# Kernel optimization log

Measured on AMD Instinct MI355X. Metric: run time of the kernel, lower is better.

## Reference

```python
import jax, jax.numpy as jnp
import numpy as np

N_NODES = 50000
N_EDGES = 800000
IN_CH = 128
HID = 128


def setup_inputs() -> dict:
    key = jax.random.key(0)
    ks = jax.random.split(key, 8)
    s = 0.05
    x = jax.random.normal(ks[0], (N_NODES, IN_CH), dtype=jnp.float32)
    edge_index = jax.random.randint(ks[1], (2, N_EDGES), 0, N_NODES, dtype=jnp.int64)
    W1l = jax.random.normal(ks[2], (IN_CH, HID), dtype=jnp.float32) * s
    W1r = jax.random.normal(ks[3], (IN_CH, HID), dtype=jnp.float32) * s
    b1 = jnp.zeros((HID,), dtype=jnp.float32)
    W2l = jax.random.normal(ks[4], (HID, HID), dtype=jnp.float32) * s
    W2r = jax.random.normal(ks[5], (HID, HID), dtype=jnp.float32) * s
    b2 = jnp.zeros((HID,), dtype=jnp.float32)
    Wout = jax.random.normal(ks[6], (HID, 2), dtype=jnp.float32) * s
    bout = jnp.zeros((2,), dtype=jnp.float32)
    return {"x": x, "edge_index": edge_index, "W1l": W1l, "W1r": W1r, "b1": b1,
            "W2l": W2l, "W2r": W2r, "b2": b2, "Wout": Wout, "bout": bout}


def _mean_aggr(h, src, dst, n_nodes):
    # mean of neighbor (source) features per destination node (PyG SAGEConv default)
    msg_sum = jax.ops.segment_sum(h[src], dst, num_segments=n_nodes)  # [N, D]
    deg = jax.ops.segment_sum(jnp.ones((src.shape[0],), dtype=h.dtype), dst,
                              num_segments=n_nodes)  # [N]
    return msg_sum / jnp.maximum(deg, 1.0)[:, None]


def _sage_conv(h, src, dst, Wl, Wr, b, n_nodes):
    aggr = _mean_aggr(h, src, dst, n_nodes)
    return aggr @ Wl + h @ Wr + b


def reference(x, edge_index, W1l, W1r, b1, W2l, W2r, b2, Wout, bout):
    n = x.shape[0]
    src, dst = edge_index[0], edge_index[1]
    h = jax.nn.relu(_sage_conv(x, src, dst, W1l, W1r, b1, n))
    # dropout is identity in inference mode
    h = jax.nn.relu(_sage_conv(h, src, dst, W2l, W2r, b2, n))
    logits = h @ Wout + bout
    return (logits, h)
```

## Files before the change

kernel.cpp:

```cpp
#include <hip/hip_runtime.h>

#define NN 50000
#define NE 800000
#define CH 128
#define CAP 64

#define NBLK 256
#define EPB (NE / NBLK)
#define HWORDS (NN / 2)

#define WTP_BLK 256
#define CAST_BLK ((NN * (CH / 2) / 4 + 255) / 256)

typedef __attribute__((ext_vector_type(8))) short short8;
typedef __attribute__((ext_vector_type(4))) float float4a;
typedef __attribute__((ext_vector_type(4))) float fltx4;
typedef __attribute__((ext_vector_type(4))) unsigned untx4;

#define DEG_OFF  0
#define CSR_OFF  50048
#define XB_OFF   1650048
#define AGB_OFF  4850048
#define H1B_OFF  8050048
#define WTP_OFF  11250048
#define BH_OFF   AGB_OFF

static __device__ __forceinline__ unsigned short f2b(float f) {
    unsigned u = __float_as_uint(f);
    unsigned r = u + 0x7fff + ((u >> 16) & 1);
    return (unsigned short)(r >> 16);
}

__global__ __launch_bounds__(256) void k_count(
    const int* __restrict__ eidx, unsigned* __restrict__ bh) {
    __shared__ unsigned h[HWORDS];
    for (int i = threadIdx.x; i < HWORDS; i += 256) h[i] = 0;
    __syncthreads();
    int b = blockIdx.x;
    const int* srcp = eidx + (size_t)b * EPB;
    const int* dstp = eidx + NE + (size_t)b * EPB;
    for (int i = threadIdx.x; i < EPB; i += 256) {
        int s = srcp[i];
        int d = dstp[i];
        if ((unsigned)d < NN && (unsigned)s < NN)
            atomicAdd(&h[d >> 1], 1u << ((d & 1) * 16));
    }
    __syncthreads();
    unsigned* out = bh + (size_t)b * HWORDS;
    for (int i = threadIdx.x; i < HWORDS; i += 256) out[i] = h[i];
}

__global__ __launch_bounds__(256) void k_scan(
    unsigned* __restrict__ bh, int* __restrict__ deg) {
    int i = blockIdx.x * 256 + threadIdx.x;
    if (i >= HWORDS) return;
    unsigned lo = 0, hi = 0;
    for (int b = 0; b < NBLK; ++b) {
        unsigned v = bh[(size_t)b * HWORDS + i];
        bh[(size_t)b * HWORDS + i] = lo | (hi << 16);
        lo += v & 0xffffu;
        hi += v >> 16;
    }
    deg[i * 2]     = (int)lo;
    deg[i * 2 + 1] = (int)hi;
}

__global__ __launch_bounds__(256) void k_place(
    const int* __restrict__ eidx, const unsigned* __restrict__ bh,
    unsigned short* __restrict__ csr) {
    __shared__ unsigned h[HWORDS];
    for (int i = threadIdx.x; i < HWORDS; i += 256) h[i] = 0;
    __syncthreads();
    int b = blockIdx.x;
    const int* srcp = eidx + (size_t)b * EPB;
    const int* dstp = eidx + NE + (size_t)b * EPB;
    const unsigned* base = bh + (size_t)b * HWORDS;
    for (int i = threadIdx.x; i < EPB; i += 256) {
        int s = srcp[i];
        int d = dstp[i];
        if ((unsigned)d < NN && (unsigned)s < NN) {
            int sh = (d & 1) * 16;
            unsigned prev = atomicAdd(&h[d >> 1], 1u << sh);
            unsigned rank = (prev >> sh) & 0xffffu;
            unsigned bs = (base[d >> 1] >> sh) & 0xffffu;
            int slot = min((int)(bs + rank), CAP - 1);
            csr[(size_t)d * CAP + slot] = (unsigned short)s;
        }
    }
}

__global__ __launch_bounds__(256) void k_prep(
    const float* __restrict__ W1l, const float* __restrict__ W1r,
    const float* __restrict__ W2l, const float* __restrict__ W2r,
    unsigned short* __restrict__ wtp,
    const float* __restrict__ x, unsigned* __restrict__ xb) {
    int b = blockIdx.x;
    if (b < WTP_BLK) {
        int i = b * 256 + threadIdx.x;
        int layer = i >> 15;
        int li = i & 32767;
        int e = li & 7, lane = (li >> 3) & 63, j = (li >> 9) & 7, kt = li >> 12;
        int ln = lane & 15, quad = lane >> 4;
        int n = j * 16 + ln;
        int k = kt * 32 + quad * 8 + e;
        const float* Wl = layer ? W2l : W1l;
        const float* Wr = layer ? W2r : W1r;
        float v = (k < 128) ? Wl[k * 128 + n] : Wr[(k - 128) * 128 + n];
        __builtin_nontemporal_store(f2b(v), &wtp[(size_t)layer * 32768 + li]);
    } else {
        int gid = (b - WTP_BLK) * 256 + threadIdx.x;
        if (gid < NN * (CH / 2) / 4) {
            fltx4 v0 = __builtin_nontemporal_load((const fltx4*)x + gid * 2);
            fltx4 v1 = __builtin_nontemporal_load((const fltx4*)x + gid * 2 + 1);
            untx4 o;
            o.x = (unsigned)f2b(v0.x) | ((unsigned)f2b(v0.y) << 16);
            o.y = (unsigned)f2b(v0.z) | ((unsigned)f2b(v0.w) << 16);
            o.z = (unsigned)f2b(v1.x) | ((unsigned)f2b(v1.y) << 16);
            o.w = (unsigned)f2b(v1.z) | ((unsigned)f2b(v1.w) << 16);
            __builtin_nontemporal_store(o, (untx4*)xb + gid);
        }
    }
}

static __device__ __forceinline__ void acc8(float* acc, uint4 v) {
    acc[0] += __uint_as_float(v.x << 16); acc[1] += __uint_as_float(v.x & 0xffff0000u);
    acc[2] += __uint_as_float(v.y << 16); acc[3] += __uint_as_float(v.y & 0xffff0000u);
    acc[4] += __uint_as_float(v.z << 16); acc[5] += __uint_as_float(v.z & 0xffff0000u);
    acc[6] += __uint_as_float(v.w << 16); acc[7] += __uint_as_float(v.w & 0xffff0000u);
}

__global__ __launch_bounds__(256) void k_gather4(
    const int* __restrict__ deg, const unsigned short* __restrict__ csr,
    const uint4* __restrict__ featb, uint4* __restrict__ aggrb) {
    int wave = (blockIdx.x * 256 + threadIdx.x) >> 6;
    int lane = threadIdx.x & 63;
    if (wave >= NN) return;
    int d = min(deg[wave], CAP);
    const unsigned short* row = csr + (size_t)wave * CAP;
    int g = lane >> 4;
    int c = lane & 15;

    float acc[8];
    #pragma unroll
    for (int e = 0; e < 8; ++e) acc[e] = 0.0f;

    int i0 = 0;
    for (; i0 + 16 <= d; i0 += 16) {
        int s1 = row[i0 + g];
        int s2 = row[i0 + 4 + g];
        int s3 = row[i0 + 8 + g];
        int s4 = row[i0 + 12 + g];
        uint4 v1 = featb[(size_t)s1 * 16 + c];
        uint4 v2 = featb[(size_t)s2 * 16 + c];
        uint4 v3 = featb[(size_t)s3 * 16 + c];
        uint4 v4 = featb[(size_t)s4 * 16 + c];
        acc8(acc, v1); acc8(acc, v2); acc8(acc, v3); acc8(acc, v4);
    }
    for (; i0 + 8 <= d; i0 += 8) {
        int s1 = row[i0 + g];
        int s2 = row[i0 + 4 + g];
        uint4 v1 = featb[(size_t)s1 * 16 + c];
        uint4 v2 = featb[(size_t)s2 * 16 + c];
        acc8(acc, v1); acc8(acc, v2);
    }
    if (i0 < d) {
        int n1 = i0 + g, n2 = i0 + 4 + g;
        int s1 = (n1 < d) ? (int)row[n1] : 0;
        int s2 = (n2 < d) ? (int)row[n2] : 0;
        uint4 v1 = featb[(size_t)s1 * 16 + c];
        uint4 v2 = featb[(size_t)s2 * 16 + c];
        if (n1 < d) acc8(acc, v1);
        if (n2 < d) acc8(acc, v2);
    }

    #pragma unroll
    for (int e = 0; e < 8; ++e) {
        acc[e] += __shfl_xor(acc[e], 32, 64);
        acc[e] += __shfl_xor(acc[e], 16, 64);
    }
    if (lane < 16) {
        float s = 1.0f / (float)(d > 1 ? d : 1);
        uint4 o;
        o.x = (unsigned)f2b(acc[0] * s) | ((unsigned)f2b(acc[1] * s) << 16);
        o.y = (unsigned)f2b(acc[2] * s) | ((unsigned)f2b(acc[3] * s) << 16);
        o.z = (unsigned)f2b(acc[4] * s) | ((unsigned)f2b(acc[5] * s) << 16);
        o.w = (unsigned)f2b(acc[6] * s) | ((unsigned)f2b(acc[7] * s) << 16);
        aggrb[(size_t)wave * 16 + c] = o;
    }
}

template <bool BF16OUT>
__global__ __launch_bounds__(256) void k_layer_mfma(
    const short* __restrict__ aggrb, const short* __restrict__ hinb,
    const short* __restrict__ wtp, const float* __restrict__ bias,
    float* __restrict__ outf, unsigned short* __restrict__ outb,
    const float* __restrict__ Wout, const float* __restrict__ bout,
    float* __restrict__ logits) {
    int lane = threadIdx.x & 63;
    int wid = threadIdx.x >> 6;
    int m0 = blockIdx.x * 64 + wid * 16;
    int ln = lane & 15;
    int quad = lane >> 4;
    int m = m0 + ln;
    int mc = min(m, NN - 1);

    float4a acc[8];
    #pragma unroll
    for (int j = 0; j < 8; ++j) acc[j] = (float4a){0.0f, 0.0f, 0.0f, 0.0f};

    #pragma unroll
    for (int kt = 0; kt < 8; ++kt) {
        const short* arow = (kt < 4 ? aggrb : hinb) + (size_t)mc * CH + (kt & 3) * 32 + quad * 8;
        short8 av = *(const short8*)arow;
        const short* bk = wtp + (size_t)kt * 4096 + lane * 8;
        #pragma unroll
        for (int j = 0; j < 8; ++j) {
            short8 bv = *(const short8*)(bk + j * 512);
            acc[j] = __builtin_amdgcn_mfma_f32_16x16x32_bf16(av, bv, acc[j], 0, 0, 0);
        }
    }

    float p0[4], p1[4];
    #pragma unroll
    for (int r = 0; r < 4; ++r) { p0[r] = 0.0f; p1[r] = 0.0f; }

    #pragma unroll
    for (int j = 0; j < 8; ++j) {
        int col = j * 16 + ln;
        float bj = bias[col];
        float w0 = 0.0f, w1 = 0.0f;
        if (!BF16OUT) { w0 = Wout[col * 2]; w1 = Wout[col * 2 + 1]; }
        #pragma unroll
        for (int r = 0; r < 4; ++r) {
            int row = m0 + quad * 4 + r;
            float v = fmaxf(acc[j][r] + bj, 0.0f);
            if (row < NN) {
                if (BF16OUT) outb[(size_t)row * CH + col] = f2b(v);
                else         outf[(size_t)row * CH + col] = v;
            }
            if (!BF16OUT) { p0[r] = fmaf(v, w0, p0[r]); p1[r] = fmaf(v, w1, p1[r]); }
        }
    }

    if (!BF16OUT) {
        #pragma unroll
        for (int r = 0; r < 4; ++r) {
            #pragma unroll
            for (int off = 1; off < 16; off <<= 1) {
                p0[r] += __shfl_xor(p0[r], off, 64);
                p1[r] += __shfl_xor(p1[r], off, 64);
            }
        }
        if (ln == 0) {
            float b0 = bout[0], b1 = bout[1];
            #pragma unroll
            for (int r = 0; r < 4; ++r) {
                int row = m0 + quad * 4 + r;
                if (row < NN) {
                    logits[row * 2 + 0] = p0[r] + b0;
                    logits[row * 2 + 1] = p1[r] + b1;
                }
            }
        }
    }
}

extern "C" void kernel_launch(void* const* d_in, const int* in_sizes, int n_in,
                              void* d_out, int out_size, void* d_ws, size_t ws_size,
                              hipStream_t stream) {
    const float* x    = (const float*)d_in[0];
    const int*   eidx = (const int*)d_in[1];
    const float* W1l  = (const float*)d_in[2];
    const float* W1r  = (const float*)d_in[3];
    const float* b1   = (const float*)d_in[4];
    const float* W2l  = (const float*)d_in[5];
    const float* W2r  = (const float*)d_in[6];
    const float* b2   = (const float*)d_in[7];
    const float* Wout = (const float*)d_in[8];
    const float* bout = (const float*)d_in[9];

    float* out    = (float*)d_out;
    float* ws     = (float*)d_ws;
    int*   deg    = (int*)ws;
    unsigned short* csr = (unsigned short*)(ws + CSR_OFF);
    unsigned* xb  = (unsigned*)(ws + XB_OFF);
    unsigned* agb = (unsigned*)(ws + AGB_OFF);
    unsigned* h1b = (unsigned*)(ws + H1B_OFF);
    unsigned* bh  = (unsigned*)(ws + BH_OFF);
    unsigned short* wtp = (unsigned short*)(ws + WTP_OFF);
    float* logits = out;
    float* hout   = out + 100000;

    k_count<<<NBLK, 256, 0, stream>>>(eidx, bh);
    k_scan<<<(HWORDS + 255) / 256, 256, 0, stream>>>(bh, deg);
    k_place<<<NBLK, 256, 0, stream>>>(eidx, bh, csr);

    k_prep<<<WTP_BLK + CAST_BLK, 256, 0, stream>>>(W1l, W1r, W2l, W2r, wtp, x, xb);

    k_gather4<<<(NN + 3) / 4, 256, 0, stream>>>(deg, csr, (const uint4*)xb, (uint4*)agb);
    k_layer_mfma<true><<<(NN + 63) / 64, 256, 0, stream>>>(
        (const short*)agb, (const short*)xb, (const short*)wtp, b1,
        nullptr, (unsigned short*)h1b, nullptr, nullptr, nullptr);

    k_gather4<<<(NN + 3) / 4, 256, 0, stream>>>(deg, csr, (const uint4*)h1b, (uint4*)agb);
    k_layer_mfma<false><<<(NN + 63) / 64, 256, 0, stream>>>(
        (const short*)agb, (const short*)h1b, (const short*)(wtp + 32768), b2,
        hout, nullptr, Wout, bout, logits);
}
```

Before: 251.1 us.

## Split column scan into two levels and store per-edge ranks for flat placement

The per-node prefix scan over 256 block histograms is split into two passes: eight groups of 32 blocks scanned in parallel, then a short scan over the group partials. This is meant to shorten the serial dependency chain of the old single-pass scan, which only launched about 98 blocks. k_count now records each edge's local rank, so k_place becomes a flat one-thread-per-edge kernel with no shared-memory histogram or atomics. In exchange it adds an extra launch, workspace for the ranks and partials, and more global reads in placement.

```diff
diff --git a/kernel.cpp b/kernel.cpp
--- a/kernel.cpp
+++ b/kernel.cpp
@@ -8,6 +8,7 @@
 #define NBLK 256
 #define EPB (NE / NBLK)
 #define HWORDS (NN / 2)
+#define NGRP 8
 
 #define WTP_BLK 256
 #define CAST_BLK ((NN * (CH / 2) / 4 + 255) / 256)
@@ -23,7 +24,9 @@
 #define AGB_OFF  4850048
 #define H1B_OFF  8050048
 #define WTP_OFF  11250048
-#define BH_OFF   AGB_OFF
+#define BH_OFF   11283456
+#define RNK_OFF  17683456
+#define PART_OFF 18083456
 
 static __device__ __forceinline__ unsigned short f2b(float f) {
     unsigned u = __float_as_uint(f);
@@ -32,32 +35,56 @@
 }
 
 __global__ __launch_bounds__(256) void k_count(
-    const int* __restrict__ eidx, unsigned* __restrict__ bh) {
+    const int* __restrict__ eidx, unsigned* __restrict__ bh,
+    unsigned short* __restrict__ rnk) {
     __shared__ unsigned h[HWORDS];
     for (int i = threadIdx.x; i < HWORDS; i += 256) h[i] = 0;
     __syncthreads();
     int b = blockIdx.x;
-    const int* srcp = eidx + (size_t)b * EPB;
-    const int* dstp = eidx + NE + (size_t)b * EPB;
+    int ebase = b * EPB;
     for (int i = threadIdx.x; i < EPB; i += 256) {
-        int s = srcp[i];
-        int d = dstp[i];
-        if ((unsigned)d < NN && (unsigned)s < NN)
-            atomicAdd(&h[d >> 1], 1u << ((d & 1) * 16));
+        int e = ebase + i;
+        int s = eidx[e];
+        int d = eidx[NE + e];
+        unsigned r = 0xffffu;
+        if ((unsigned)d < NN && (unsigned)s < NN) {
+            int sh = (d & 1) * 16;
+            unsigned prev = atomicAdd(&h[d >> 1], 1u << sh);
+            r = (prev >> sh) & 0xffffu;
+        }
+        rnk[e] = (unsigned short)r;
     }
     __syncthreads();
     unsigned* out = bh + (size_t)b * HWORDS;
     for (int i = threadIdx.x; i < HWORDS; i += 256) out[i] = h[i];
 }
 
-__global__ __launch_bounds__(256) void k_scan(
-    unsigned* __restrict__ bh, int* __restrict__ deg) {
+__global__ __launch_bounds__(256) void k_scanA(
+    unsigned* __restrict__ bh, unsigned* __restrict__ part) {
+    int i = blockIdx.x * 256 + threadIdx.x;
+    if (i >= HWORDS) return;
+    int g = blockIdx.y;
+    unsigned lo = 0, hi = 0;
+    size_t base = (size_t)g * 32 * HWORDS + i;
+    #pragma unroll 4
+    for (int b = 0; b < 32; ++b) {
+        unsigned v = bh[base + (size_t)b * HWORDS];
+        bh[base + (size_t)b * HWORDS] = lo | (hi << 16);
+        lo += v & 0xffffu;
+        hi += v >> 16;
+    }
+    part[(size_t)g * HWORDS + i] = lo | (hi << 16);
+}
+
+__global__ __launch_bounds__(256) void k_scanB(
+    unsigned* __restrict__ part, int* __restrict__ deg) {
     int i = blockIdx.x * 256 + threadIdx.x;
     if (i >= HWORDS) return;
     unsigned lo = 0, hi = 0;
-    for (int b = 0; b < NBLK; ++b) {
-        unsigned v = bh[(size_t)b * HWORDS + i];
-        bh[(size_t)b * HWORDS + i] = lo | (hi << 16);
+    #pragma unroll
+    for (int g = 0; g < NGRP; ++g) {
+        unsigned v = part[(size_t)g * HWORDS + i];
+        part[(size_t)g * HWORDS + i] = lo | (hi << 16);
         lo += v & 0xffffu;
         hi += v >> 16;
     }
@@ -67,26 +94,20 @@
 
 __global__ __launch_bounds__(256) void k_place(
     const int* __restrict__ eidx, const unsigned* __restrict__ bh,
+    const unsigned* __restrict__ part, const unsigned short* __restrict__ rnk,
     unsigned short* __restrict__ csr) {
-    __shared__ unsigned h[HWORDS];
-    for (int i = threadIdx.x; i < HWORDS; i += 256) h[i] = 0;
-    __syncthreads();
-    int b = blockIdx.x;
-    const int* srcp = eidx + (size_t)b * EPB;
-    const int* dstp = eidx + NE + (size_t)b * EPB;
-    const unsigned* base = bh + (size_t)b * HWORDS;
-    for (int i = threadIdx.x; i < EPB; i += 256) {
-        int s = srcp[i];
-        int d = dstp[i];
-        if ((unsigned)d < NN && (unsigned)s < NN) {
-            int sh = (d & 1) * 16;
-            unsigned prev = atomicAdd(&h[d >> 1], 1u << sh);
-            unsigned rank = (prev >> sh) & 0xffffu;
-            unsigned bs = (base[d >> 1] >> sh) & 0xffffu;
-            int slot = min((int)(bs + rank), CAP - 1);
-            csr[(size_t)d * CAP + slot] = (unsigned short)s;
-        }
-    }
+    int e = blockIdx.x * 256 + threadIdx.x;
+    if (e >= NE) return;
+    int s = eidx[e];
+    int d = eidx[NE + e];
+    if ((unsigned)d >= NN || (unsigned)s >= NN) return;
+    int b = e / EPB;
+    int sh = (d & 1) * 16;
+    unsigned lb = (bh[(size_t)b * HWORDS + (d >> 1)] >> sh) & 0xffffu;
+    unsigned gb = (part[(size_t)(b >> 5) * HWORDS + (d >> 1)] >> sh) & 0xffffu;
+    unsigned r = rnk[e];
+    int slot = min((int)(gb + lb + r), CAP - 1);
+    csr[(size_t)d * CAP + slot] = (unsigned short)s;
 }
 
 __global__ __launch_bounds__(256) void k_prep(
@@ -286,14 +307,18 @@
     unsigned* xb  = (unsigned*)(ws + XB_OFF);
     unsigned* agb = (unsigned*)(ws + AGB_OFF);
     unsigned* h1b = (unsigned*)(ws + H1B_OFF);
+    unsigned short* wtp = (unsigned short*)(ws + WTP_OFF);
     unsigned* bh  = (unsigned*)(ws + BH_OFF);
-    unsigned short* wtp = (unsigned short*)(ws + WTP_OFF);
+    unsigned short* rnk = (unsigned short*)(ws + RNK_OFF);
+    unsigned* part = (unsigned*)(ws + PART_OFF);
     float* logits = out;
     float* hout   = out + 100000;
 
-    k_count<<<NBLK, 256, 0, stream>>>(eidx, bh);
-    k_scan<<<(HWORDS + 255) / 256, 256, 0, stream>>>(bh, deg);
-    k_place<<<NBLK, 256, 0, stream>>>(eidx, bh, csr);
+    k_count<<<NBLK, 256, 0, stream>>>(eidx, bh, rnk);
+    dim3 sgrid((HWORDS + 255) / 256, NGRP);
+    k_scanA<<<sgrid, 256, 0, stream>>>(bh, part);
+    k_scanB<<<(HWORDS + 255) / 256, 256, 0, stream>>>(part, deg);
+    k_place<<<(NE + 255) / 256, 256, 0, stream>>>(eidx, bh, part, rnk, csr);
 
     k_prep<<<WTP_BLK + CAST_BLK, 256, 0, stream>>>(W1l, W1r, W2l, W2r, wtp, x, xb);
 
```

After: 248.1 us. Within noise of the previous version (-1.2%).

## Fuse gather into MFMA layer kernel and restructure CSR build with stored ranks

Applied to the files above, without the earlier changes.

The neighbor mean-aggregation is fused into the MFMA layer kernel. Each wave gathers 16 rows into LDS and the block then runs the GEMM from LDS, so the aggregated bf16 buffer never goes to global memory and two launches disappear. CSR construction now records per-edge ranks in the count pass, which lets the place step run as a flat per-edge pass merged with the weight and x prep kernel. The histogram block count drops from 256 to 64, cutting scan traffic at the cost of less count parallelism. The risk is that fused blocks cover only 64 nodes with serial per-wave gathers, which may limit occupancy and latency hiding.

```diff
diff --git a/kernel.cpp b/kernel.cpp
--- a/kernel.cpp
+++ b/kernel.cpp
@@ -5,12 +5,13 @@
 #define CH 128
 #define CAP 64
 
-#define NBLK 256
+#define NBLK 64
 #define EPB (NE / NBLK)
 #define HWORDS (NN / 2)
 
+#define PLACE_BLK (NE / 256)
 #define WTP_BLK 256
-#define CAST_BLK ((NN * (CH / 2) / 4 + 255) / 256)
+#define CAST_BLK (NN * (CH / 2) / 4 / 256)
 
 typedef __attribute__((ext_vector_type(8))) short short8;
 typedef __attribute__((ext_vector_type(4))) float float4a;
@@ -20,10 +21,10 @@
 #define DEG_OFF  0
 #define CSR_OFF  50048
 #define XB_OFF   1650048
-#define AGB_OFF  4850048
-#define H1B_OFF  8050048
-#define WTP_OFF  11250048
-#define BH_OFF   AGB_OFF
+#define H1B_OFF  4850048
+#define WTP_OFF  8050048
+#define BH_OFF   8083456
+#define RNK_OFF  9683456
 
 static __device__ __forceinline__ unsigned short f2b(float f) {
     unsigned u = __float_as_uint(f);
@@ -32,18 +33,24 @@
 }
 
 __global__ __launch_bounds__(256) void k_count(
-    const int* __restrict__ eidx, unsigned* __restrict__ bh) {
+    const int* __restrict__ eidx, unsigned* __restrict__ bh,
+    unsigned short* __restrict__ rnk) {
     __shared__ unsigned h[HWORDS];
     for (int i = threadIdx.x; i < HWORDS; i += 256) h[i] = 0;
     __syncthreads();
     int b = blockIdx.x;
-    const int* srcp = eidx + (size_t)b * EPB;
-    const int* dstp = eidx + NE + (size_t)b * EPB;
+    int ebase = b * EPB;
     for (int i = threadIdx.x; i < EPB; i += 256) {
-        int s = srcp[i];
-        int d = dstp[i];
-        if ((unsigned)d < NN && (unsigned)s < NN)
-            atomicAdd(&h[d >> 1], 1u << ((d & 1) * 16));
+        int e = ebase + i;
+        int s = eidx[e];
+        int d = eidx[NE + e];
+        unsigned r = 0xffffu;
+        if ((unsigned)d < NN && (unsigned)s < NN) {
+            int sh = (d & 1) * 16;
+            unsigned prev = atomicAdd(&h[d >> 1], 1u << sh);
+            r = (prev >> sh) & 0xffffu;
+        }
+        rnk[e] = (unsigned short)r;
     }
     __syncthreads();
     unsigned* out = bh + (size_t)b * HWORDS;
@@ -55,48 +62,37 @@
     int i = blockIdx.x * 256 + threadIdx.x;
     if (i >= HWORDS) return;
     unsigned lo = 0, hi = 0;
+    #pragma unroll 8
     for (int b = 0; b < NBLK; ++b) {
         unsigned v = bh[(size_t)b * HWORDS + i];
         bh[(size_t)b * HWORDS + i] = lo | (hi << 16);
         lo += v & 0xffffu;
         hi += v >> 16;
     }
-    deg[i * 2]     = (int)lo;
-    deg[i * 2 + 1] = (int)hi;
-}
-
-__global__ __launch_bounds__(256) void k_place(
+    int2 o; o.x = (int)lo; o.y = (int)hi;
+    *(int2*)&deg[i * 2] = o;
+}
+
+__global__ __launch_bounds__(256) void k_place_prep(
     const int* __restrict__ eidx, const unsigned* __restrict__ bh,
-    unsigned short* __restrict__ csr) {
-    __shared__ unsigned h[HWORDS];
-    for (int i = threadIdx.x; i < HWORDS; i += 256) h[i] = 0;
-    __syncthreads();
-    int b = blockIdx.x;
-    const int* srcp = eidx + (size_t)b * EPB;
-    const int* dstp = eidx + NE + (size_t)b * EPB;
-    const unsigned* base = bh + (size_t)b * HWORDS;
-    for (int i = threadIdx.x; i < EPB; i += 256) {
-        int s = srcp[i];
-        int d = dstp[i];
-        if ((unsigned)d < NN && (unsigned)s < NN) {
-            int sh = (d & 1) * 16;
-            unsigned prev = atomicAdd(&h[d >> 1], 1u << sh);
-            unsigned rank = (prev >> sh) & 0xffffu;
-            unsigned bs = (base[d >> 1] >> sh) & 0xffffu;
-            int slot = min((int)(bs + rank), CAP - 1);
-            csr[(size_t)d * CAP + slot] = (unsigned short)s;
-        }
-    }
-}
-
-__global__ __launch_bounds__(256) void k_prep(
+    const unsigned short* __restrict__ rnk, unsigned short* __restrict__ csr,
     const float* __restrict__ W1l, const float* __restrict__ W1r,
     const float* __restrict__ W2l, const float* __restrict__ W2r,
     unsigned short* __restrict__ wtp,
     const float* __restrict__ x, unsigned* __restrict__ xb) {
     int b = blockIdx.x;
-    if (b < WTP_BLK) {
-        int i = b * 256 + threadIdx.x;
+    if (b < PLACE_BLK) {
+        int e = b * 256 + threadIdx.x;
+        int s = eidx[e];
+        int d = eidx[NE + e];
+        if ((unsigned)d >= NN || (unsigned)s >= NN) return;
+        int blk = e / EPB;
+        int sh = (d & 1) * 16;
+        unsigned base = (bh[(size_t)blk * HWORDS + (d >> 1)] >> sh) & 0xffffu;
+        int slot = min((int)(base + rnk[e]), CAP - 1);
+        csr[(size_t)d * CAP + slot] = (unsigned short)s;
+    } else if (b < PLACE_BLK + WTP_BLK) {
+        int i = (b - PLACE_BLK) * 256 + threadIdx.x;
         int layer = i >> 15;
         int li = i & 32767;
         int e = li & 7, lane = (li >> 3) & 63, j = (li >> 9) & 7, kt = li >> 12;
@@ -108,7 +104,7 @@
         float v = (k < 128) ? Wl[k * 128 + n] : Wr[(k - 128) * 128 + n];
         __builtin_nontemporal_store(f2b(v), &wtp[(size_t)layer * 32768 + li]);
     } else {
-        int gid = (b - WTP_BLK) * 256 + threadIdx.x;
+        int gid = (b - PLACE_BLK - WTP_BLK) * 256 + threadIdx.x;
         if (gid < NN * (CH / 2) / 4) {
             fltx4 v0 = __builtin_nontemporal_load((const fltx4*)x + gid * 2);
             fltx4 v1 = __builtin_nontemporal_load((const fltx4*)x + gid * 2 + 1);
@@ -129,80 +125,84 @@
     acc[6] += __uint_as_float(v.w << 16); acc[7] += __uint_as_float(v.w & 0xffff0000u);
 }
 
-__global__ __launch_bounds__(256) void k_gather4(
+template <bool BF16OUT>
+__global__ __launch_bounds__(256) void k_fused(
     const int* __restrict__ deg, const unsigned short* __restrict__ csr,
-    const uint4* __restrict__ featb, uint4* __restrict__ aggrb) {
-    int wave = (blockIdx.x * 256 + threadIdx.x) >> 6;
-    int lane = threadIdx.x & 63;
-    if (wave >= NN) return;
-    int d = min(deg[wave], CAP);
-    const unsigned short* row = csr + (size_t)wave * CAP;
-    int g = lane >> 4;
-    int c = lane & 15;
-
-    float acc[8];
-    #pragma unroll
-    for (int e = 0; e < 8; ++e) acc[e] = 0.0f;
-
-    int i0 = 0;
-    for (; i0 + 16 <= d; i0 += 16) {
-        int s1 = row[i0 + g];
-        int s2 = row[i0 + 4 + g];
-        int s3 = row[i0 + 8 + g];
-        int s4 = row[i0 + 12 + g];
-        uint4 v1 = featb[(size_t)s1 * 16 + c];
-        uint4 v2 = featb[(size_t)s2 * 16 + c];
-        uint4 v3 = featb[(size_t)s3 * 16 + c];
-        uint4 v4 = featb[(size_t)s4 * 16 + c];
-        acc8(acc, v1); acc8(acc, v2); acc8(acc, v3); acc8(acc, v4);
-    }
-    for (; i0 + 8 <= d; i0 += 8) {
-        int s1 = row[i0 + g];
-        int s2 = row[i0 + 4 + g];
-        uint4 v1 = featb[(size_t)s1 * 16 + c];
-        uint4 v2 = featb[(size_t)s2 * 16 + c];
-        acc8(acc, v1); acc8(acc, v2);
-    }
-    if (i0 < d) {
-        int n1 = i0 + g, n2 = i0 + 4 + g;
-        int s1 = (n1 < d) ? (int)row[n1] : 0;
-        int s2 = (n2 < d) ? (int)row[n2] : 0;
-        uint4 v1 = featb[(size_t)s1 * 16 + c];
-        uint4 v2 = featb[(size_t)s2 * 16 + c];
-        if (n1 < d) acc8(acc, v1);
-        if (n2 < d) acc8(acc, v2);
-    }
-
-    #pragma unroll
-    for (int e = 0; e < 8; ++e) {
-        acc[e] += __shfl_xor(acc[e], 32, 64);
-        acc[e] += __shfl_xor(acc[e], 16, 64);
-    }
-    if (lane < 16) {
-        float s = 1.0f / (float)(d > 1 ? d : 1);
-        uint4 o;
-        o.x = (unsigned)f2b(acc[0] * s) | ((unsigned)f2b(acc[1] * s) << 16);
-        o.y = (unsigned)f2b(acc[2] * s) | ((unsigned)f2b(acc[3] * s) << 16);
-        o.z = (unsigned)f2b(acc[4] * s) | ((unsigned)f2b(acc[5] * s) << 16);
-        o.w = (unsigned)f2b(acc[6] * s) | ((unsigned)f2b(acc[7] * s) << 16);
-        aggrb[(size_t)wave * 16 + c] = o;
-    }
-}
-
-template <bool BF16OUT>
-__global__ __launch_bounds__(256) void k_layer_mfma(
-    const short* __restrict__ aggrb, const short* __restrict__ hinb,
-    const short* __restrict__ wtp, const float* __restrict__ bias,
+    const uint4* __restrict__ featb, const short* __restrict__ wtp,
+    const float* __restrict__ bias,
     float* __restrict__ outf, unsigned short* __restrict__ outb,
     const float* __restrict__ Wout, const float* __restrict__ bout,
     float* __restrict__ logits) {
+    __shared__ unsigned lds_a[64][68];
+    int w = threadIdx.x >> 6;
     int lane = threadIdx.x & 63;
-    int wid = threadIdx.x >> 6;
-    int m0 = blockIdx.x * 64 + wid * 16;
+    int m0 = blockIdx.x * 64;
+    int g = lane >> 4;
+    int c = lane & 15;
+
+    for (int i = 0; i < 16; ++i) {
+        int n = m0 + w * 16 + i;
+        int nc = min(n, NN - 1);
+        int d = (n < NN) ? min(deg[nc], CAP) : 0;
+        const unsigned short* row = csr + (size_t)nc * CAP;
+
+        float acc[8];
+        #pragma unroll
+        for (int e = 0; e < 8; ++e) acc[e] = 0.0f;
+
+        int i0 = 0;
+        for (; i0 + 16 <= d; i0 += 16) {
+            int s1 = row[i0 + g];
+            int s2 = row[i0 + 4 + g];
+            int s3 = row[i0 + 8 + g];
+            int s4 = row[i0 + 12 + g];
+            uint4 v1 = featb[(size_t)s1 * 16 + c];
+            uint4 v2 = featb[(size_t)s2 * 16 + c];
+            uint4 v3 = featb[(size_t)s3 * 16 + c];
+            uint4 v4 = featb[(size_t)s4 * 16 + c];
+            acc8(acc, v1); acc8(acc, v2); acc8(acc, v3); acc8(acc, v4);
+        }
+        for (; i0 + 8 <= d; i0 += 8) {
+            int s1 = row[i0 + g];
+            int s2 = row[i0 + 4 + g];
+            uint4 v1 = featb[(size_t)s1 * 16 + c];
+            uint4 v2 = featb[(size_t)s2 * 16 + c];
+            acc8(acc, v1); acc8(acc, v2);
+        }
+        if (i0 < d) {
+            int n1 = i0 + g, n2 = i0 + 4 + g;
+            int s1 = (n1 < d) ? (int)row[n1] : 0;
+            int s2 = (n2 < d) ? (int)row[n2] : 0;
+            uint4 v1 = featb[(size_t)s1 * 16 + c];
+            uint4 v2 = featb[(size_t)s2 * 16 + c];
+            if (n1 < d) acc8(acc, v1);
+            if (n2 < d) acc8(acc, v2);
+        }
+
+        #pragma unroll
+        for (int e = 0; e < 8; ++e) {
+            acc[e] += __shfl_xor(acc[e], 32, 64);
+            acc[e] += __shfl_xor(acc[e], 16, 64);
+        }
+        if (lane < 16) {
+            float s = 1.0f / (float)(d > 1 ? d : 1);
+            uint4 o;
+            o.x = (unsigned)f2b(acc[0] * s) | ((unsigned)f2b(acc[1] * s) << 16);
+            o.y = (unsigned)f2b(acc[2] * s) | ((unsigned)f2b(acc[3] * s) << 16);
+            o.z = (unsigned)f2b(acc[4] * s) | ((unsigned)f2b(acc[5] * s) << 16);
+            o.w = (unsigned)f2b(acc[6] * s) | ((unsigned)f2b(acc[7] * s) << 16);
+            *(uint4*)&lds_a[w * 16 + i][c * 4] = o;
+        }
+    }
+    __syncthreads();
+
+    int wid = w;
+    int mrow0 = m0 + wid * 16;
     int ln = lane & 15;
     int quad = lane >> 4;
-    int m = m0 + ln;
+    int m = mrow0 + ln;
     int mc = min(m, NN - 1);
+    int lr = wid * 16 + ln;
 
     float4a acc[8];
     #pragma unroll
@@ -210,8 +210,13 @@
 
     #pragma unroll
     for (int kt = 0; kt < 8; ++kt) {
-        const short* arow = (kt < 4 ? aggrb : hinb) + (size_t)mc * CH + (kt & 3) * 32 + quad * 8;
-        short8 av = *(const short8*)arow;
+        short8 av;
+        if (kt < 4) {
+            av = *(const short8*)&lds_a[lr][kt * 16 + quad * 4];
+        } else {
+            const short* arow = (const short*)featb + (size_t)mc * CH + (kt & 3) * 32 + quad * 8;
+            av = *(const short8*)arow;
+        }
         const short* bk = wtp + (size_t)kt * 4096 + lane * 8;
         #pragma unroll
         for (int j = 0; j < 8; ++j) {
@@ -232,7 +237,7 @@
         if (!BF16OUT) { w0 = Wout[col * 2]; w1 = Wout[col * 2 + 1]; }
         #pragma unroll
         for (int r = 0; r < 4; ++r) {
-            int row = m0 + quad * 4 + r;
+            int row = mrow0 + quad * 4 + r;
             float v = fmaxf(acc[j][r] + bj, 0.0f);
             if (row < NN) {
                 if (BF16OUT) outb[(size_t)row * CH + col] = f2b(v);
@@ -255,7 +260,7 @@
             float b0 = bout[0], b1 = bout[1];
             #pragma unroll
             for (int r = 0; r < 4; ++r) {
-                int row = m0 + quad * 4 + r;
+                int row = mrow0 + quad * 4 + r;
                 if (row < NN) {
                     logits[row * 2 + 0] = p0[r] + b0;
                     logits[row * 2 + 1] = p1[r] + b1;
@@ -284,26 +289,23 @@
     int*   deg    = (int*)ws;
     unsigned short* csr = (unsigned short*)(ws + CSR_OFF);
     unsigned* xb  = (unsigned*)(ws + XB_OFF);
-    unsigned* agb = (unsigned*)(ws + AGB_OFF);
     unsigned* h1b = (unsigned*)(ws + H1B_OFF);
+    unsigned short* wtp = (unsigned short*)(ws + WTP_OFF);
     unsigned* bh  = (unsigned*)(ws + BH_OFF);
-    unsigned short* wtp = (unsigned short*)(ws + WTP_OFF);
+    unsigned short* rnk = (unsigned short*)(ws + RNK_OFF);
     float* logits = out;
     float* hout   = out + 100000;
 
-    k_count<<<NBLK, 256, 0, stream>>>(eidx, bh);
+    k_count<<<NBLK, 256, 0, stream>>>(eidx, bh, rnk);
     k_scan<<<(HWORDS + 255) / 256, 256, 0, stream>>>(bh, deg);
-    k_place<<<NBLK, 256, 0, stream>>>(eidx, bh, csr);
-
-    k_prep<<<WTP_BLK + CAST_BLK, 256, 0, stream>>>(W1l, W1r, W2l, W2r, wtp, x, xb);
-
-    k_gather4<<<(NN + 3) / 4, 256, 0, stream>>>(deg, csr, (const uint4*)xb, (uint4*)agb);
-    k_layer_mfma<true><<<(NN + 63) / 64, 256, 0, stream>>>(
-        (const short*)agb, (const short*)xb, (const short*)wtp, b1,
+    k_place_prep<<<PLACE_BLK + WTP_BLK + CAST_BLK, 256, 0, stream>>>(
+        eidx, bh, rnk, csr, W1l, W1r, W2l, W2r, wtp, x, xb);
+
+    k_fused<true><<<(NN + 63) / 64, 256, 0, stream>>>(
+        deg, csr, (const uint4*)xb, (const short*)wtp, b1,
         nullptr, (unsigned short*)h1b, nullptr, nullptr, nullptr);
 
-    k_gather4<<<(NN + 3) / 4, 256, 0, stream>>>(deg, csr, (const uint4*)h1b, (uint4*)agb);
-    k_layer_mfma<false><<<(NN + 63) / 64, 256, 0, stream>>>(
-        (const short*)agb, (const short*)h1b, (const short*)(wtp + 32768), b2,
+    k_fused<false><<<(NN + 63) / 64, 256, 0, stream>>>(
+        deg, csr, (const uint4*)h1b, (const short*)(wtp + 32768), b2,
         hout, nullptr, Wout, bout, logits);
 }
```

Result: slower. 283.4 us (+12.9%).
